# Performance work log

Measured on AMD Instinct MI355X. Metric: run time of the kernel, lower is better.

The kernel has to match this reference:

```python
import jax, jax.numpy as jnp
import numpy as np

K_PRED = 6
TEMP = 0.8  # score_temperature
MTR_THRESH = [3.5, 1.0, 1.75]  # meters per type [veh, ped, cyc]
MPA_THRESH = [2.5, 1.0, 1.5]


def _within(xy, thresh):
    # xy: [S, A, P, T, 2], thresh: [S, A] -> bool [S, A, P, P]; ADE(i, j) < thresh (use_ade=True)
    diff = xy[:, :, None, :, :, :] - xy[:, :, :, None, :, :]  # [S, A, P, P, T, 2]
    ade = jnp.sqrt((diff * diff).sum(-1)).mean(-1)            # [S, A, P, P]
    return ade < thresh[:, :, None, None]


def _mtr_nms(trajs, scores, agent_type):
    # Greedy sequential top-k with distance-based down-weighting (MTR-style NMS).
    thresh = agent_type @ jnp.asarray(MTR_THRESH, scores.dtype)  # [S, A]
    within = _within(trajs[..., :2], thresh)                     # [S, A, P, P]
    P = scores.shape[-1]

    def step(carry, _):
        idx = jnp.argmax(carry, axis=-1)                                              # [S, A]
        row = jnp.take_along_axis(within, idx[:, :, None, None], axis=2)[:, :, 0, :]  # [S, A, P]
        carry = carry * ((~row).astype(carry.dtype) * 0.99 + 0.01)
        carry = jnp.where(jnp.arange(P) == idx[:, :, None], -1.0, carry)
        return carry, idx

    _, mode_idx = jax.lax.scan(step, scores, None, length=K_PRED)  # [K, S, A]
    mode_idx = jnp.moveaxis(mode_idx, 0, -1)                       # [S, A, K]
    trajs_k = jnp.take_along_axis(trajs, mode_idx[:, :, :, None, None], axis=2)
    scores_k = jnp.take_along_axis(scores, mode_idx, axis=2)
    return trajs_k, scores_k / scores_k.sum(-1, keepdims=True)


def _mpa_nms(valid, trajs, scores, agent_type):
    # Sequential suppression in descending-score order; mode k drops to 0.001 if any
    # nearby mode currently has a higher score. Faithful to the torch nested loop.
    thresh = agent_type @ jnp.asarray(MPA_THRESH, scores.dtype)  # [S, A]
    within = _within(trajs[..., :2], thresh)                     # [S, A, K, K]

    def per_agent(w, s, v):
        order = jnp.argsort(-s)  # descending score order

        def step(carry, k):
            suppress = jnp.any(w[k] & (carry > carry[k]))
            carry = carry.at[k].set(jnp.where(v & suppress, jnp.asarray(0.001, carry.dtype), carry[k]))
            return carry, None

        out, _ = jax.lax.scan(step, s, order)
        return out

    s = jax.vmap(jax.vmap(per_agent))(within, scores, valid)
    return s / s.sum(-1, keepdims=True)


def forward(valid, scores, trajs, agent_type):
    scores = scores / scores.sum(-1, keepdims=True)
    S, A, P, T, D = trajs.shape
    # n_pred > k_pred, aggr_thresh=[], mtr_nms_thresh non-empty -> mtr_nms branch
    trajs_k, scores_k = _mtr_nms(trajs, scores, agent_type)
    # mpa_nms_thresh non-empty -> mpa_nms
    scores_k = _mpa_nms(valid, trajs_k, scores_k, agent_type)
    # score_temperature > 0
    scores_k = jax.nn.softmax(jnp.log(scores_k) / TEMP, axis=-1)
    tr = jnp.transpose(trajs_k, (0, 3, 1, 2, 4))  # movedim(3,1): [S, T, A, K, D]
    waymo_trajs = tr[..., :2]
    waymo_yaw_bbox = tr[..., 2:3]
    waymo_spd = tr[..., 3:4]
    waymo_valid = jnp.broadcast_to(valid[:, None, :], (S, T, A))
    return waymo_trajs, waymo_yaw_bbox, waymo_spd, scores_k, waymo_valid


def setup_inputs():
    key = jax.random.key(0)
    k1, k2, k3, k4, k5 = jax.random.split(key, 5)
    S, A, P, T = 8, 64, 32, 80
    valid = jax.random.bernoulli(k1, 0.9, (S, A))
    scores = jax.random.uniform(k2, (S, A, P), minval=0.01, maxval=1.0)
    # shared base path + per-mode noise so pairwise ADEs straddle the NMS thresholds
    base = jax.random.normal(k3, (S, A, 1, T, 4)) * 20.0
    trajs = base + jax.random.normal(k4, (S, A, P, T, 4)) * 1.5
    agent_type = jax.nn.one_hot(jax.random.randint(k5, (S, A), 0, 3), 3, dtype=jnp.float32)
    return {"valid": valid, "scores": scores, "trajs": trajs, "agent_type": agent_type}


def reference(valid, scores, trajs, agent_type):
    return forward(valid, scores, trajs, agent_type)
```

## Files before the change

kernel.cpp:

```cpp
#include <hip/hip_runtime.h>
#include <math.h>
#include <float.h>

#define NS 8
#define NA 64
#define NP 32
#define NT 80
#define NK 6
#define NAG (NS*NA)
#define PAIRS 496

#define FSQRT(x) __builtin_amdgcn_sqrtf(x)

#define BASE1 ((size_t)NS*NT*NA*NK*2)
#define BASE2 (BASE1 + (size_t)NS*NT*NA*NK)
#define BASE3 (BASE2 + (size_t)NS*NT*NA*NK)
#define BASE4 (BASE3 + (size_t)NS*NA*NK)

__global__ __launch_bounds__(512) void k_fused(
    const void* __restrict__ valid_raw,
    const float* __restrict__ scores,
    const float* __restrict__ trajs,
    const float* __restrict__ atype,
    float* __restrict__ out)
{
    const int bid = blockIdx.x;
    const int blk = (bid & 7) * 64 + (bid >> 3);
    const int s = blk >> 6;
    const int a = blk & 63;
    const int tid = threadIdx.x;
    const int lane = tid & 63;
    const int p = lane & 31;

    __shared__ float2 sxy[NT][NP + 1];
    __shared__ float sade[NP][NP];
    __shared__ unsigned wloc[NP];

    if (tid < NP) wloc[tid] = 1u << tid;

    const unsigned* vw = (const unsigned*)valid_raw;
    unsigned u0 = vw[lane], u1 = vw[lane + 64];
    float sc = scores[blk*NP + p];
    const float a0 = atype[blk*3+0], a1 = atype[blk*3+1], a2 = atype[blk*3+2];
    const float thrM = a0*3.5f + a1*1.0f + a2*1.75f;
    const float thrQ = a0*2.5f + a1*1.0f + a2*1.5f;

    const float4* tg4 = (const float4*)trajs + (size_t)blk * NP * NT;
    #pragma unroll
    for (int rep = 0; rep < 5; ++rep) {
        int l = tid + rep*512;
        int pp = l / NT, t = l - pp*NT;
        float4 v = tg4[l];
        sxy[t][pp] = make_float2(v.x, v.y);
    }
    __syncthreads();

    {
        const int tile = tid >> 2, slice = tid & 3;
        int A_, B_, C_, D_;
        bool offd = (tile < 120);
        if (offd) {
            float fs = sqrtf((float)(1 + 8*tile));
            int tj = (int)((1.0f + fs) * 0.5f);
            int ti = tile - ((tj*(tj-1)) >> 1);
            A_ = 2*ti; B_ = 2*ti+1; C_ = 2*tj; D_ = 2*tj+1;
        } else {
            int m = tile - 120;
            A_ = 4*m; B_ = 4*m+2; C_ = 4*m+1; D_ = 4*m+3;
        }
        float accAC = 0.0f, accAD = 0.0f, accBC = 0.0f, accBD = 0.0f;
        const int tbase = slice * 20;
        #pragma unroll 4
        for (int tt = 0; tt < 20; ++tt) {
            int t = tbase + tt;
            float2 va = sxy[t][A_], vb = sxy[t][B_];
            float2 vc = sxy[t][C_], vd = sxy[t][D_];
            float dx, dy;
            dx = va.x - vc.x; dy = va.y - vc.y; accAC += FSQRT(fmaf(dx,dx,dy*dy));
            dx = va.x - vd.x; dy = va.y - vd.y; accAD += FSQRT(fmaf(dx,dx,dy*dy));
            dx = vb.x - vc.x; dy = vb.y - vc.y; accBC += FSQRT(fmaf(dx,dx,dy*dy));
            dx = vb.x - vd.x; dy = vb.y - vd.y; accBD += FSQRT(fmaf(dx,dx,dy*dy));
        }
        const int qb = lane & ~3;
#define FOLD(acc) ((((acc) + __shfl((acc), qb+1)) + __shfl((acc), qb+2)) + __shfl((acc), qb+3))
        float fAC = FOLD(accAC);
        float fAD = FOLD(accAD);
        float fBC = FOLD(accBC);
        float fBD = FOLD(accBD);
#undef FOLD
        if (slice == 0) {
            const float inv = 1.0f / (float)NT;
            float e0 = fAC*inv, e1 = fAD*inv, e2 = fBC*inv, e3 = fBD*inv;
            sade[A_][C_] = e0; sade[C_][A_] = e0;
            if (e0 < thrM) { atomicOr(&wloc[A_], 1u<<C_); atomicOr(&wloc[C_], 1u<<A_); }
            sade[B_][D_] = e3; sade[D_][B_] = e3;
            if (e3 < thrM) { atomicOr(&wloc[B_], 1u<<D_); atomicOr(&wloc[D_], 1u<<B_); }
            if (offd) {
                sade[A_][D_] = e1; sade[D_][A_] = e1;
                if (e1 < thrM) { atomicOr(&wloc[A_], 1u<<D_); atomicOr(&wloc[D_], 1u<<A_); }
                sade[B_][C_] = e2; sade[C_][B_] = e2;
                if (e2 < thrM) { atomicOr(&wloc[B_], 1u<<C_); atomicOr(&wloc[C_], 1u<<B_); }
            }
        }
    }
    __syncthreads();

    bool fHit = (u0 == 0x3F800000u) || (u1 == 0x3F800000u);
    int nz0 = ((u0&0xFFu)!=0)+((u0&0xFF00u)!=0)+((u0&0xFF0000u)!=0)+((u0&0xFF000000u)!=0);
    int nz1 = ((u1&0xFFu)!=0)+((u1&0xFF00u)!=0)+((u1&0xFF0000u)!=0)+((u1&0xFF000000u)!=0);
    bool isF = __any(fHit), multi = __any(nz0 >= 2 || nz1 >= 2);
    int vflag;
    if (isF)        vflag = (((const float*)valid_raw)[blk] != 0.0f);
    else if (multi) vflag = (((const unsigned char*)valid_raw)[blk] != 0);
    else            vflag = (((const int*)valid_raw)[blk] != 0);

    unsigned wl = wloc[p];

    float carry = sc;
    int sel_0, sel_1, sel_2, sel_3, sel_4, sel_5;
#define GREEDY(SK) { \
    float vv = carry; \
    _Pragma("unroll") \
    for (int off = 16; off; off >>= 1) vv = fmaxf(vv, __shfl_xor(vv, off)); \
    unsigned long long mba = __ballot(carry == vv); \
    int bi = __ffsll((long long)mba) - 1; \
    SK = bi; \
    unsigned rbi = __shfl(wl, bi); \
    carry = (p == bi) ? -1.0f : (((rbi >> p) & 1u) ? carry*0.01f : carry); }
    GREEDY(sel_0) GREEDY(sel_1) GREEDY(sel_2) GREEDY(sel_3) GREEDY(sel_4) GREEDY(sel_5)
#undef GREEDY

    float q0 = __shfl(sc, sel_0), q1 = __shfl(sc, sel_1), q2 = __shfl(sc, sel_2);
    float q3 = __shfl(sc, sel_3), q4 = __shfl(sc, sel_4), q5 = __shfl(sc, sel_5);

    int ii = (lane<5)?0 : (lane<9)?1 : (lane<12)?2 : (lane<14)?3 : 4;
    int jj = lane - ((ii==0)?-1 : (ii==1)?3 : (ii==2)?6 : (ii==3)?8 : 9);
    jj = (jj < 0) ? 0 : (jj > 5 ? 5 : jj);
    int pi = (ii==0)?sel_0:(ii==1)?sel_1:(ii==2)?sel_2:(ii==3)?sel_3:(ii==4)?sel_4:sel_5;
    int pj = (jj==0)?sel_0:(jj==1)?sel_1:(jj==2)?sel_2:(jj==3)?sel_3:(jj==4)?sel_4:sel_5;
    float ade15 = sade[pi][pj];
    bool within = (lane < 15) && (ade15 < thrQ);
    unsigned long long bal = __ballot(within);
#define B(i) ((unsigned)((bal >> (i)) & 1ull))
    unsigned w6_0 = (B(0)<<1)|(B(1)<<2)|(B(2)<<3)|(B(3)<<4)|(B(4)<<5);
    unsigned w6_1 = (B(0)<<0)|(B(5)<<2)|(B(6)<<3)|(B(7)<<4)|(B(8)<<5);
    unsigned w6_2 = (B(1)<<0)|(B(5)<<1)|(B(9)<<3)|(B(10)<<4)|(B(11)<<5);
    unsigned w6_3 = (B(2)<<0)|(B(6)<<1)|(B(9)<<2)|(B(12)<<4)|(B(13)<<5);
    unsigned w6_4 = (B(3)<<0)|(B(7)<<1)|(B(10)<<2)|(B(12)<<3)|(B(14)<<5);
    unsigned w6_5 = (B(4)<<0)|(B(8)<<1)|(B(11)<<2)|(B(13)<<3)|(B(14)<<4);
#undef B

#define GE(x,y) ((x) >= (y))
    bool a01=GE(q0,q1), a02=GE(q0,q2), a03=GE(q0,q3), a04=GE(q0,q4), a05=GE(q0,q5);
    bool a12=GE(q1,q2), a13=GE(q1,q3), a14=GE(q1,q4), a15=GE(q1,q5);
    bool a23=GE(q2,q3), a24=GE(q2,q4), a25=GE(q2,q5);
    bool a34=GE(q3,q4), a35=GE(q3,q5);
    bool a45=GE(q4,q5);
#undef GE
    int r0 = (!a01)+(!a02)+(!a03)+(!a04)+(!a05);
    int r1 = a01+(!a12)+(!a13)+(!a14)+(!a15);
    int r2 = a02+a12+(!a23)+(!a24)+(!a25);
    int r3 = a03+a13+a23+(!a34)+(!a35);
    int r4 = a04+a14+a24+a34+(!a45);
    int r5 = a05+a15+a25+a35+a45;

    const float sum6 = q0+q1+q2+q3+q4+q5;
    const float supv = 0.001f * sum6;
#define STEP(m) { \
    float ck = (r0==m)?q0:(r1==m)?q1:(r2==m)?q2:(r3==m)?q3:(r4==m)?q4:q5; \
    unsigned wk = (r0==m)?w6_0:(r1==m)?w6_1:(r2==m)?w6_2:(r3==m)?w6_3:(r4==m)?w6_4:w6_5; \
    bool sup = (((wk>>0)&1u)&&(q0>ck))||(((wk>>1)&1u)&&(q1>ck))||(((wk>>2)&1u)&&(q2>ck)) \
             ||(((wk>>3)&1u)&&(q3>ck))||(((wk>>4)&1u)&&(q4>ck))||(((wk>>5)&1u)&&(q5>ck)); \
    bool go = vflag && sup; \
    q0 = (go&&(r0==m))?supv:q0; q1 = (go&&(r1==m))?supv:q1; q2 = (go&&(r2==m))?supv:q2; \
    q3 = (go&&(r3==m))?supv:q3; q4 = (go&&(r4==m))?supv:q4; q5 = (go&&(r5==m))?supv:q5; }
    STEP(0) STEP(1) STEP(2) STEP(3) STEP(4) STEP(5)
#undef STEP

    float g0 = __logf(q0)*1.25f, g1 = __logf(q1)*1.25f, g2 = __logf(q2)*1.25f;
    float g3 = __logf(q3)*1.25f, g4 = __logf(q4)*1.25f, g5 = __logf(q5)*1.25f;
    float mx = fmaxf(fmaxf(fmaxf(g0,g1),fmaxf(g2,g3)),fmaxf(g4,g5));
    float e0 = __expf(g0-mx), e1 = __expf(g1-mx), e2 = __expf(g2-mx);
    float e3 = __expf(g3-mx), e4 = __expf(g4-mx), e5 = __expf(g5-mx);
    float es = e0+e1+e2+e3+e4+e5;

    if (tid < NK) {
        float fv = (lane==0)?e0:(lane==1)?e1:(lane==2)?e2:(lane==3)?e3:(lane==4)?e4:e5;
        out[BASE3 + (size_t)blk*NK + lane] = fv / es;
    }
    if (tid < NT)
        out[BASE4 + (size_t)(s*NT + tid)*NA + a] = vflag ? 1.0f : 0.0f;

    if (tid < 3*NT) {
        int t = tid / 3, kp = tid - t*3;
        int k0 = kp*2;
        int s0sel = (kp==0)?sel_0:(kp==1)?sel_2:sel_4;
        int s1sel = (kp==0)?sel_1:(kp==1)?sel_3:sel_5;
        float4 v0 = tg4[(size_t)s0sel*NT + t];
        float4 v1 = tg4[(size_t)s1sel*NT + t];
        size_t ob = (((size_t)(s*NT + t)*NA + a)*NK + k0);
        *(float4*)((float2*)out + ob) = make_float4(v0.x, v0.y, v1.x, v1.y);
        *(float2*)(out + BASE1 + ob) = make_float2(v0.z, v1.z);
        *(float2*)(out + BASE2 + ob) = make_float2(v0.w, v1.w);
    }
}

extern "C" void kernel_launch(void* const* d_in, const int* in_sizes, int n_in,
                              void* d_out, int out_size, void* d_ws, size_t ws_size,
                              hipStream_t stream) {
    const void*  valid  = d_in[0];
    const float* scores = (const float*)d_in[1];
    const float* trajs  = (const float*)d_in[2];
    const float* atype  = (const float*)d_in[3];
    k_fused<<<NAG, 512, 0, stream>>>(valid, scores, trajs, atype, (float*)d_out);
}
```

Measured before the change: 18.97 us.

## Use 4x4 register tiles for pairwise ADE and restrict post-phase to four waves

Replaces the 2x2 pairwise-distance tiling over 496 pairs with 4x4 register tiles (28 off-diagonal plus 8 diagonal groups), loaded as float4 from a repacked shared array. Only 144 threads compute distances, and the greedy and MPA tail runs on the first 256 threads. This raises data reuse per shared-memory load and trims redundant work in unused waves. The cost is lower parallelism and more registers in the distance phase, which may lengthen its critical path.

```diff
diff --git a/kernel.cpp b/kernel.cpp
--- a/kernel.cpp
+++ b/kernel.cpp
@@ -8,9 +8,13 @@
 #define NT 80
 #define NK 6
 #define NAG (NS*NA)
-#define PAIRS 496
 
 #define FSQRT(x) __builtin_amdgcn_sqrtf(x)
+
+__device__ __forceinline__ float pdist(float ax, float ay, float bx, float by) {
+    float dx = ax - bx, dy = ay - by;
+    return FSQRT(fmaf(dx, dx, dy*dy));
+}
 
 #define BASE1 ((size_t)NS*NT*NA*NK*2)
 #define BASE2 (BASE1 + (size_t)NS*NT*NA*NK)
@@ -32,7 +36,7 @@
     const int lane = tid & 63;
     const int p = lane & 31;
 
-    __shared__ float2 sxy[NT][NP + 1];
+    __shared__ float4 s4[NT][17];
     __shared__ float sade[NP][NP];
     __shared__ unsigned wloc[NP];
 
@@ -51,157 +55,185 @@
         int l = tid + rep*512;
         int pp = l / NT, t = l - pp*NT;
         float4 v = tg4[l];
-        sxy[t][pp] = make_float2(v.x, v.y);
+        ((float2*)&s4[t][0])[pp] = make_float2(v.x, v.y);
     }
     __syncthreads();
 
-    {
+    if (tid < 144) {
         const int tile = tid >> 2, slice = tid & 3;
-        int A_, B_, C_, D_;
-        bool offd = (tile < 120);
-        if (offd) {
+        const int tbase = slice * 20;
+        const int qb = lane & ~3;
+        const float inv = 1.0f / (float)NT;
+#define FOLD(acc) ((((acc) + __shfl((acc), qb+1)) + __shfl((acc), qb+2)) + __shfl((acc), qb+3))
+#define EMIT(F, I, J) { float ade = (F)*inv; sade[I][J] = ade; sade[J][I] = ade; \
+        if (ade < thrM) { atomicOr(&wloc[I], 1u<<(J)); atomicOr(&wloc[J], 1u<<(I)); } }
+        if (tile < 28) {
             float fs = sqrtf((float)(1 + 8*tile));
-            int tj = (int)((1.0f + fs) * 0.5f);
-            int ti = tile - ((tj*(tj-1)) >> 1);
-            A_ = 2*ti; B_ = 2*ti+1; C_ = 2*tj; D_ = 2*tj+1;
+            int gj = (int)((1.0f + fs) * 0.5f);
+            int gi = tile - ((gj*(gj-1)) >> 1);
+            const int bi4 = 4*gi, bj4 = 4*gj;
+            float c00=0,c01=0,c02=0,c03=0, c10=0,c11=0,c12=0,c13=0;
+            float c20=0,c21=0,c22=0,c23=0, c30=0,c31=0,c32=0,c33=0;
+            for (int tt = 0; tt < 20; ++tt) {
+                int t = tbase + tt;
+                float4 fa0 = s4[t][2*gi], fa1 = s4[t][2*gi+1];
+                float4 fb0 = s4[t][2*gj], fb1 = s4[t][2*gj+1];
+                c00 += pdist(fa0.x,fa0.y, fb0.x,fb0.y);
+                c01 += pdist(fa0.x,fa0.y, fb0.z,fb0.w);
+                c02 += pdist(fa0.x,fa0.y, fb1.x,fb1.y);
+                c03 += pdist(fa0.x,fa0.y, fb1.z,fb1.w);
+                c10 += pdist(fa0.z,fa0.w, fb0.x,fb0.y);
+                c11 += pdist(fa0.z,fa0.w, fb0.z,fb0.w);
+                c12 += pdist(fa0.z,fa0.w, fb1.x,fb1.y);
+                c13 += pdist(fa0.z,fa0.w, fb1.z,fb1.w);
+                c20 += pdist(fa1.x,fa1.y, fb0.x,fb0.y);
+                c21 += pdist(fa1.x,fa1.y, fb0.z,fb0.w);
+                c22 += pdist(fa1.x,fa1.y, fb1.x,fb1.y);
+                c23 += pdist(fa1.x,fa1.y, fb1.z,fb1.w);
+                c30 += pdist(fa1.z,fa1.w, fb0.x,fb0.y);
+                c31 += pdist(fa1.z,fa1.w, fb0.z,fb0.w);
+                c32 += pdist(fa1.z,fa1.w, fb1.x,fb1.y);
+                c33 += pdist(fa1.z,fa1.w, fb1.z,fb1.w);
+            }
+            float f00=FOLD(c00), f01=FOLD(c01), f02=FOLD(c02), f03=FOLD(c03);
+            float f10=FOLD(c10), f11=FOLD(c11), f12=FOLD(c12), f13=FOLD(c13);
+            float f20=FOLD(c20), f21=FOLD(c21), f22=FOLD(c22), f23=FOLD(c23);
+            float f30=FOLD(c30), f31=FOLD(c31), f32=FOLD(c32), f33=FOLD(c33);
+            if (slice == 0) {
+                EMIT(f00, bi4+0, bj4+0) EMIT(f01, bi4+0, bj4+1)
+                EMIT(f02, bi4+0, bj4+2) EMIT(f03, bi4+0, bj4+3)
+                EMIT(f10, bi4+1, bj4+0) EMIT(f11, bi4+1, bj4+1)
+                EMIT(f12, bi4+1, bj4+2) EMIT(f13, bi4+1, bj4+3)
+                EMIT(f20, bi4+2, bj4+0) EMIT(f21, bi4+2, bj4+1)
+                EMIT(f22, bi4+2, bj4+2) EMIT(f23, bi4+2, bj4+3)
+                EMIT(f30, bi4+3, bj4+0) EMIT(f31, bi4+3, bj4+1)
+                EMIT(f32, bi4+3, bj4+2) EMIT(f33, bi4+3, bj4+3)
+            }
         } else {
-            int m = tile - 120;
-            A_ = 4*m; B_ = 4*m+2; C_ = 4*m+1; D_ = 4*m+3;
+            const int g = tile - 28;
+            const int b4 = 4*g;
+            float d01=0,d02=0,d03=0,d12=0,d13=0,d23=0;
+            for (int tt = 0; tt < 20; ++tt) {
+                int t = tbase + tt;
+                float4 fa0 = s4[t][2*g], fa1 = s4[t][2*g+1];
+                d01 += pdist(fa0.x,fa0.y, fa0.z,fa0.w);
+                d02 += pdist(fa0.x,fa0.y, fa1.x,fa1.y);
+                d03 += pdist(fa0.x,fa0.y, fa1.z,fa1.w);
+                d12 += pdist(fa0.z,fa0.w, fa1.x,fa1.y);
+                d13 += pdist(fa0.z,fa0.w, fa1.z,fa1.w);
+                d23 += pdist(fa1.x,fa1.y, fa1.z,fa1.w);
+            }
+            float g01=FOLD(d01), g02=FOLD(d02), g03=FOLD(d03);
+            float g12=FOLD(d12), g13=FOLD(d13), g23=FOLD(d23);
+            if (slice == 0) {
+                EMIT(g01, b4+0, b4+1) EMIT(g02, b4+0, b4+2) EMIT(g03, b4+0, b4+3)
+                EMIT(g12, b4+1, b4+2) EMIT(g13, b4+1, b4+3) EMIT(g23, b4+2, b4+3)
+            }
         }
-        float accAC = 0.0f, accAD = 0.0f, accBC = 0.0f, accBD = 0.0f;
-        const int tbase = slice * 20;
-        #pragma unroll 4
-        for (int tt = 0; tt < 20; ++tt) {
-            int t = tbase + tt;
-            float2 va = sxy[t][A_], vb = sxy[t][B_];
-            float2 vc = sxy[t][C_], vd = sxy[t][D_];
-            float dx, dy;
-            dx = va.x - vc.x; dy = va.y - vc.y; accAC += FSQRT(fmaf(dx,dx,dy*dy));
-            dx = va.x - vd.x; dy = va.y - vd.y; accAD += FSQRT(fmaf(dx,dx,dy*dy));
-            dx = vb.x - vc.x; dy = vb.y - vc.y; accBC += FSQRT(fmaf(dx,dx,dy*dy));
-            dx = vb.x - vd.x; dy = vb.y - vd.y; accBD += FSQRT(fmaf(dx,dx,dy*dy));
-        }
-        const int qb = lane & ~3;
-#define FOLD(acc) ((((acc) + __shfl((acc), qb+1)) + __shfl((acc), qb+2)) + __shfl((acc), qb+3))
-        float fAC = FOLD(accAC);
-        float fAD = FOLD(accAD);
-        float fBC = FOLD(accBC);
-        float fBD = FOLD(accBD);
+#undef EMIT
 #undef FOLD
-        if (slice == 0) {
-            const float inv = 1.0f / (float)NT;
-            float e0 = fAC*inv, e1 = fAD*inv, e2 = fBC*inv, e3 = fBD*inv;
-            sade[A_][C_] = e0; sade[C_][A_] = e0;
-            if (e0 < thrM) { atomicOr(&wloc[A_], 1u<<C_); atomicOr(&wloc[C_], 1u<<A_); }
-            sade[B_][D_] = e3; sade[D_][B_] = e3;
-            if (e3 < thrM) { atomicOr(&wloc[B_], 1u<<D_); atomicOr(&wloc[D_], 1u<<B_); }
-            if (offd) {
-                sade[A_][D_] = e1; sade[D_][A_] = e1;
-                if (e1 < thrM) { atomicOr(&wloc[A_], 1u<<D_); atomicOr(&wloc[D_], 1u<<A_); }
-                sade[B_][C_] = e2; sade[C_][B_] = e2;
-                if (e2 < thrM) { atomicOr(&wloc[B_], 1u<<C_); atomicOr(&wloc[C_], 1u<<B_); }
-            }
-        }
     }
     __syncthreads();
 
-    bool fHit = (u0 == 0x3F800000u) || (u1 == 0x3F800000u);
-    int nz0 = ((u0&0xFFu)!=0)+((u0&0xFF00u)!=0)+((u0&0xFF0000u)!=0)+((u0&0xFF000000u)!=0);
-    int nz1 = ((u1&0xFFu)!=0)+((u1&0xFF00u)!=0)+((u1&0xFF0000u)!=0)+((u1&0xFF000000u)!=0);
-    bool isF = __any(fHit), multi = __any(nz0 >= 2 || nz1 >= 2);
-    int vflag;
-    if (isF)        vflag = (((const float*)valid_raw)[blk] != 0.0f);
-    else if (multi) vflag = (((const unsigned char*)valid_raw)[blk] != 0);
-    else            vflag = (((const int*)valid_raw)[blk] != 0);
-
-    unsigned wl = wloc[p];
-
-    float carry = sc;
-    int sel_0, sel_1, sel_2, sel_3, sel_4, sel_5;
+    if (tid < 256) {
+        bool fHit = (u0 == 0x3F800000u) || (u1 == 0x3F800000u);
+        int nz0 = ((u0&0xFFu)!=0)+((u0&0xFF00u)!=0)+((u0&0xFF0000u)!=0)+((u0&0xFF000000u)!=0);
+        int nz1 = ((u1&0xFFu)!=0)+((u1&0xFF00u)!=0)+((u1&0xFF0000u)!=0)+((u1&0xFF000000u)!=0);
+        bool isF = __any(fHit), multi = __any(nz0 >= 2 || nz1 >= 2);
+        int vflag;
+        if (isF)        vflag = (((const float*)valid_raw)[blk] != 0.0f);
+        else if (multi) vflag = (((const unsigned char*)valid_raw)[blk] != 0);
+        else            vflag = (((const int*)valid_raw)[blk] != 0);
+
+        unsigned wl = wloc[p];
+
+        float carry = sc;
+        int sel_0, sel_1, sel_2, sel_3, sel_4, sel_5;
 #define GREEDY(SK) { \
-    float vv = carry; \
-    _Pragma("unroll") \
-    for (int off = 16; off; off >>= 1) vv = fmaxf(vv, __shfl_xor(vv, off)); \
-    unsigned long long mba = __ballot(carry == vv); \
-    int bi = __ffsll((long long)mba) - 1; \
-    SK = bi; \
-    unsigned rbi = __shfl(wl, bi); \
-    carry = (p == bi) ? -1.0f : (((rbi >> p) & 1u) ? carry*0.01f : carry); }
-    GREEDY(sel_0) GREEDY(sel_1) GREEDY(sel_2) GREEDY(sel_3) GREEDY(sel_4) GREEDY(sel_5)
+        float vv = carry; \
+        _Pragma("unroll") \
+        for (int off = 16; off; off >>= 1) vv = fmaxf(vv, __shfl_xor(vv, off)); \
+        unsigned long long mba = __ballot(carry == vv); \
+        int bi = __ffsll((long long)mba) - 1; \
+        SK = bi; \
+        unsigned rbi = __shfl(wl, bi); \
+        carry = (p == bi) ? -1.0f : (((rbi >> p) & 1u) ? carry*0.01f : carry); }
+        GREEDY(sel_0) GREEDY(sel_1) GREEDY(sel_2) GREEDY(sel_3) GREEDY(sel_4) GREEDY(sel_5)
 #undef GREEDY
 
-    float q0 = __shfl(sc, sel_0), q1 = __shfl(sc, sel_1), q2 = __shfl(sc, sel_2);
-    float q3 = __shfl(sc, sel_3), q4 = __shfl(sc, sel_4), q5 = __shfl(sc, sel_5);
-
-    int ii = (lane<5)?0 : (lane<9)?1 : (lane<12)?2 : (lane<14)?3 : 4;
-    int jj = lane - ((ii==0)?-1 : (ii==1)?3 : (ii==2)?6 : (ii==3)?8 : 9);
-    jj = (jj < 0) ? 0 : (jj > 5 ? 5 : jj);
-    int pi = (ii==0)?sel_0:(ii==1)?sel_1:(ii==2)?sel_2:(ii==3)?sel_3:(ii==4)?sel_4:sel_5;
-    int pj = (jj==0)?sel_0:(jj==1)?sel_1:(jj==2)?sel_2:(jj==3)?sel_3:(jj==4)?sel_4:sel_5;
-    float ade15 = sade[pi][pj];
-    bool within = (lane < 15) && (ade15 < thrQ);
-    unsigned long long bal = __ballot(within);
+        float q0 = __shfl(sc, sel_0), q1 = __shfl(sc, sel_1), q2 = __shfl(sc, sel_2);
+        float q3 = __shfl(sc, sel_3), q4 = __shfl(sc, sel_4), q5 = __shfl(sc, sel_5);
+
+        int ii = (lane<5)?0 : (lane<9)?1 : (lane<12)?2 : (lane<14)?3 : 4;
+        int jj = lane - ((ii==0)?-1 : (ii==1)?3 : (ii==2)?6 : (ii==3)?8 : 9);
+        jj = (jj < 0) ? 0 : (jj > 5 ? 5 : jj);
+        int pi = (ii==0)?sel_0:(ii==1)?sel_1:(ii==2)?sel_2:(ii==3)?sel_3:(ii==4)?sel_4:sel_5;
+        int pj = (jj==0)?sel_0:(jj==1)?sel_1:(jj==2)?sel_2:(jj==3)?sel_3:(jj==4)?sel_4:sel_5;
+        float ade15 = sade[pi][pj];
+        bool within = (lane < 15) && (ade15 < thrQ);
+        unsigned long long bal = __ballot(within);
 #define B(i) ((unsigned)((bal >> (i)) & 1ull))
-    unsigned w6_0 = (B(0)<<1)|(B(1)<<2)|(B(2)<<3)|(B(3)<<4)|(B(4)<<5);
-    unsigned w6_1 = (B(0)<<0)|(B(5)<<2)|(B(6)<<3)|(B(7)<<4)|(B(8)<<5);
-    unsigned w6_2 = (B(1)<<0)|(B(5)<<1)|(B(9)<<3)|(B(10)<<4)|(B(11)<<5);
-    unsigned w6_3 = (B(2)<<0)|(B(6)<<1)|(B(9)<<2)|(B(12)<<4)|(B(13)<<5);
-    unsigned w6_4 = (B(3)<<0)|(B(7)<<1)|(B(10)<<2)|(B(12)<<3)|(B(14)<<5);
-    unsigned w6_5 = (B(4)<<0)|(B(8)<<1)|(B(11)<<2)|(B(13)<<3)|(B(14)<<4);
+        unsigned w6_0 = (B(0)<<1)|(B(1)<<2)|(B(2)<<3)|(B(3)<<4)|(B(4)<<5);
+        unsigned w6_1 = (B(0)<<0)|(B(5)<<2)|(B(6)<<3)|(B(7)<<4)|(B(8)<<5);
+        unsigned w6_2 = (B(1)<<0)|(B(5)<<1)|(B(9)<<3)|(B(10)<<4)|(B(11)<<5);
+        unsigned w6_3 = (B(2)<<0)|(B(6)<<1)|(B(9)<<2)|(B(12)<<4)|(B(13)<<5);
+        unsigned w6_4 = (B(3)<<0)|(B(7)<<1)|(B(10)<<2)|(B(12)<<3)|(B(14)<<5);
+        unsigned w6_5 = (B(4)<<0)|(B(8)<<1)|(B(11)<<2)|(B(13)<<3)|(B(14)<<4);
 #undef B
 
 #define GE(x,y) ((x) >= (y))
-    bool a01=GE(q0,q1), a02=GE(q0,q2), a03=GE(q0,q3), a04=GE(q0,q4), a05=GE(q0,q5);
-    bool a12=GE(q1,q2), a13=GE(q1,q3), a14=GE(q1,q4), a15=GE(q1,q5);
-    bool a23=GE(q2,q3), a24=GE(q2,q4), a25=GE(q2,q5);
-    bool a34=GE(q3,q4), a35=GE(q3,q5);
-    bool a45=GE(q4,q5);
+        bool a01=GE(q0,q1), a02=GE(q0,q2), a03=GE(q0,q3), a04=GE(q0,q4), a05=GE(q0,q5);
+        bool a12=GE(q1,q2), a13=GE(q1,q3), a14=GE(q1,q4), a15=GE(q1,q5);
+        bool a23=GE(q2,q3), a24=GE(q2,q4), a25=GE(q2,q5);
+        bool a34=GE(q3,q4), a35=GE(q3,q5);
+        bool a45=GE(q4,q5);
 #undef GE
-    int r0 = (!a01)+(!a02)+(!a03)+(!a04)+(!a05);
-    int r1 = a01+(!a12)+(!a13)+(!a14)+(!a15);
-    int r2 = a02+a12+(!a23)+(!a24)+(!a25);
-    int r3 = a03+a13+a23+(!a34)+(!a35);
-    int r4 = a04+a14+a24+a34+(!a45);
-    int r5 = a05+a15+a25+a35+a45;
-
-    const float sum6 = q0+q1+q2+q3+q4+q5;
-    const float supv = 0.001f * sum6;
+        int r0 = (!a01)+(!a02)+(!a03)+(!a04)+(!a05);
+        int r1 = a01+(!a12)+(!a13)+(!a14)+(!a15);
+        int r2 = a02+a12+(!a23)+(!a24)+(!a25);
+        int r3 = a03+a13+a23+(!a34)+(!a35);
+        int r4 = a04+a14+a24+a34+(!a45);
+        int r5 = a05+a15+a25+a35+a45;
+
+        const float sum6 = q0+q1+q2+q3+q4+q5;
+        const float supv = 0.001f * sum6;
 #define STEP(m) { \
-    float ck = (r0==m)?q0:(r1==m)?q1:(r2==m)?q2:(r3==m)?q3:(r4==m)?q4:q5; \
-    unsigned wk = (r0==m)?w6_0:(r1==m)?w6_1:(r2==m)?w6_2:(r3==m)?w6_3:(r4==m)?w6_4:w6_5; \
-    bool sup = (((wk>>0)&1u)&&(q0>ck))||(((wk>>1)&1u)&&(q1>ck))||(((wk>>2)&1u)&&(q2>ck)) \
-             ||(((wk>>3)&1u)&&(q3>ck))||(((wk>>4)&1u)&&(q4>ck))||(((wk>>5)&1u)&&(q5>ck)); \
-    bool go = vflag && sup; \
-    q0 = (go&&(r0==m))?supv:q0; q1 = (go&&(r1==m))?supv:q1; q2 = (go&&(r2==m))?supv:q2; \
-    q3 = (go&&(r3==m))?supv:q3; q4 = (go&&(r4==m))?supv:q4; q5 = (go&&(r5==m))?supv:q5; }
-    STEP(0) STEP(1) STEP(2) STEP(3) STEP(4) STEP(5)
+        float ck = (r0==m)?q0:(r1==m)?q1:(r2==m)?q2:(r3==m)?q3:(r4==m)?q4:q5; \
+        unsigned wk = (r0==m)?w6_0:(r1==m)?w6_1:(r2==m)?w6_2:(r3==m)?w6_3:(r4==m)?w6_4:w6_5; \
+        bool sup = (((wk>>0)&1u)&&(q0>ck))||(((wk>>1)&1u)&&(q1>ck))||(((wk>>2)&1u)&&(q2>ck)) \
+                 ||(((wk>>3)&1u)&&(q3>ck))||(((wk>>4)&1u)&&(q4>ck))||(((wk>>5)&1u)&&(q5>ck)); \
+        bool go = vflag && sup; \
+        q0 = (go&&(r0==m))?supv:q0; q1 = (go&&(r1==m))?supv:q1; q2 = (go&&(r2==m))?supv:q2; \
+        q3 = (go&&(r3==m))?supv:q3; q4 = (go&&(r4==m))?supv:q4; q5 = (go&&(r5==m))?supv:q5; }
+        STEP(0) STEP(1) STEP(2) STEP(3) STEP(4) STEP(5)
 #undef STEP
 
-    float g0 = __logf(q0)*1.25f, g1 = __logf(q1)*1.25f, g2 = __logf(q2)*1.25f;
-    float g3 = __logf(q3)*1.25f, g4 = __logf(q4)*1.25f, g5 = __logf(q5)*1.25f;
-    float mx = fmaxf(fmaxf(fmaxf(g0,g1),fmaxf(g2,g3)),fmaxf(g4,g5));
-    float e0 = __expf(g0-mx), e1 = __expf(g1-mx), e2 = __expf(g2-mx);
-    float e3 = __expf(g3-mx), e4 = __expf(g4-mx), e5 = __expf(g5-mx);
-    float es = e0+e1+e2+e3+e4+e5;
-
-    if (tid < NK) {
-        float fv = (lane==0)?e0:(lane==1)?e1:(lane==2)?e2:(lane==3)?e3:(lane==4)?e4:e5;
-        out[BASE3 + (size_t)blk*NK + lane] = fv / es;
-    }
-    if (tid < NT)
-        out[BASE4 + (size_t)(s*NT + tid)*NA + a] = vflag ? 1.0f : 0.0f;
-
-    if (tid < 3*NT) {
-        int t = tid / 3, kp = tid - t*3;
-        int k0 = kp*2;
-        int s0sel = (kp==0)?sel_0:(kp==1)?sel_2:sel_4;
-        int s1sel = (kp==0)?sel_1:(kp==1)?sel_3:sel_5;
-        float4 v0 = tg4[(size_t)s0sel*NT + t];
-        float4 v1 = tg4[(size_t)s1sel*NT + t];
-        size_t ob = (((size_t)(s*NT + t)*NA + a)*NK + k0);
-        *(float4*)((float2*)out + ob) = make_float4(v0.x, v0.y, v1.x, v1.y);
-        *(float2*)(out + BASE1 + ob) = make_float2(v0.z, v1.z);
-        *(float2*)(out + BASE2 + ob) = make_float2(v0.w, v1.w);
+        float g0 = __logf(q0)*1.25f, g1 = __logf(q1)*1.25f, g2 = __logf(q2)*1.25f;
+        float g3 = __logf(q3)*1.25f, g4 = __logf(q4)*1.25f, g5 = __logf(q5)*1.25f;
+        float mx = fmaxf(fmaxf(fmaxf(g0,g1),fmaxf(g2,g3)),fmaxf(g4,g5));
+        float e0 = __expf(g0-mx), e1 = __expf(g1-mx), e2 = __expf(g2-mx);
+        float e3 = __expf(g3-mx), e4 = __expf(g4-mx), e5 = __expf(g5-mx);
+        float es = e0+e1+e2+e3+e4+e5;
+
+        if (tid < NK) {
+            float fv = (lane==0)?e0:(lane==1)?e1:(lane==2)?e2:(lane==3)?e3:(lane==4)?e4:e5;
+            out[BASE3 + (size_t)blk*NK + lane] = fv / es;
+        }
+        if (tid < NT)
+            out[BASE4 + (size_t)(s*NT + tid)*NA + a] = vflag ? 1.0f : 0.0f;
+
+        if (tid < 3*NT) {
+            int t = tid / 3, kp = tid - t*3;
+            int k0 = kp*2;
+            int s0sel = (kp==0)?sel_0:(kp==1)?sel_2:sel_4;
+            int s1sel = (kp==0)?sel_1:(kp==1)?sel_3:sel_5;
+            float4 v0 = tg4[(size_t)s0sel*NT + t];
+            float4 v1 = tg4[(size_t)s1sel*NT + t];
+            size_t ob = (((size_t)(s*NT + t)*NA + a)*NK + k0);
+            *(float4*)((float2*)out + ob) = make_float4(v0.x, v0.y, v1.x, v1.y);
+            *(float2*)(out + BASE1 + ob) = make_float2(v0.z, v1.z);
+            *(float2*)(out + BASE2 + ob) = make_float2(v0.w, v1.w);
+        }
     }
 }
 
```

After: 22.19 us. 16.9% more time.
